# Kernel optimization log

Hardware: AMD Instinct MI355X
Metric: run time of the kernel (lower is better)

Reference implementation:

```python
import jax, jax.numpy as jnp
import numpy as np

N, D, N_SIGMAS = 4096, 128, 75

def _pairwise_sq_dist(x):
    # squared euclidean distances, [N, N]
    sq = jnp.sum(x * x, axis=1)
    d2 = sq[:, None] + sq[None, :] - 2.0 * (x @ x.T)
    return jnp.maximum(d2, 0.0)

def setup_inputs() -> dict:
    key = jax.random.key(0)
    kx, ky = jax.random.split(key)
    x = jax.random.normal(kx, (N, D), dtype=jnp.float32)
    # realistic label kernel: RBF over random 10-dim label embeddings
    y = jax.random.normal(ky, (N, 10), dtype=jnp.float32)
    label_kernel = jnp.exp(-_pairwise_sq_dist(y))
    return {"x": x, "label_kernel": label_kernel}

def reference(x, label_kernel):
    n = x.shape[0]
    d2 = _pairwise_sq_dist(x)              # [N, N] squared distances
    nz = d2 > 0
    # safe sqrt (avoid nan grads on diagonal zeros)
    dist = jnp.where(nz, jnp.sqrt(jnp.where(nz, d2, 1.0)), 0.0)
    # mean of nonzero distances (distance[distance != 0].mean())
    mean_distance = jnp.sum(dist) / jnp.sum(nz).astype(x.dtype)
    lo = 0.1 * mean_distance
    hi = 10.0 * mean_distance
    step = (hi - lo) / N_SIGMAS
    sigmas = lo + step * jnp.arange(N_SIGMAS, dtype=x.dtype)  # np.arange equivalent

    label_norm = jnp.linalg.norm(label_kernel)

    def alignment_loss(sigma):
        K = jnp.exp(-d2 / (sigma * sigma))
        return jnp.sum(K * label_kernel) / (jnp.linalg.norm(K) * label_norm)

    losses = jax.lax.map(alignment_loss, sigmas)   # sequential sigma sweep
    sigma_opt = sigmas[jnp.argmax(losses)]         # first max, like np.argwhere(...).item()

    A = jnp.exp(-d2 / (sigma_opt * sigma_opt)) / n
    return A
```

## Files before the change

kernel.cpp:

```cpp
#include <hip/hip_runtime.h>
#include <hip/hip_bf16.h>

#define NN 4096
#define DD 128
#define NS 75

#define BT 128
#define NBD2 (NN / BT)
#define GRID_D2 (NBD2 * (NBD2 + 1) / 2)

#define SB 64
#define NBSW (NN / SB)
#define NTILES (NBSW * (NBSW + 1) / 2)
#define GRID_SW (NTILES / 2)

typedef float v2f __attribute__((ext_vector_type(2)));
typedef float f32x4 __attribute__((ext_vector_type(4)));
typedef short bf16x8 __attribute__((ext_vector_type(8)));

__device__ __forceinline__ float fexp2(float v) { return __builtin_amdgcn_exp2f(v); }

__device__ __forceinline__ void gload_lds16(const void* g, void* l) {
    __builtin_amdgcn_global_load_lds(
        (const __attribute__((address_space(1))) unsigned int*)g,
        (__attribute__((address_space(3))) unsigned int*)l,
        16, 0, 0);
}

template <int CTRL>
__device__ __forceinline__ float dpp_add(float x) {
    int y = __builtin_amdgcn_update_dpp(0, __float_as_int(x), CTRL, 0xf, 0xf, true);
    return x + __int_as_float(y);
}
__device__ __forceinline__ float wave_sum(float x) {
    x = dpp_add<0x111>(x);
    x = dpp_add<0x112>(x);
    x = dpp_add<0x114>(x);
    x = dpp_add<0x118>(x);
    x = dpp_add<0x142>(x);
    x = dpp_add<0x143>(x);
    return x;
}

__device__ __forceinline__ void tri_decode(int t, int nb, int& bi, int& bj) {
    int b = 0, rem = t;
    while (rem >= nb - b) { rem -= nb - b; ++b; }
    bi = b; bj = b + rem;
}

__device__ __forceinline__ void cvt_split(const float4& v0, const float4& v1,
                                          bf16x8& hi, bf16x8& lo) {
    float f[8] = {v0.x, v0.y, v0.z, v0.w, v1.x, v1.y, v1.z, v1.w};
#pragma unroll
    for (int j = 0; j < 8; ++j) {
        unsigned b = __float_as_uint(f[j]);
        hi[j] = (short)(b >> 16);
        float l = f[j] - __uint_as_float(b & 0xFFFF0000u);
        lo[j] = (short)(__float_as_uint(l) >> 16);
    }
}

__device__ __forceinline__ int coarse_window(const double* KL, const double* KK) {
    double best = -1.0;
    int bk = 0;
    for (int k = 0; k < 25; ++k) {
        double loss = KL[k] / sqrt(KK[k]);
        if (loss > best) { best = loss; bk = k; }
    }
    int wv = 3 * bk - 2;
    if (wv < 0) wv = 0;
    if (wv > NS - 5) wv = NS - 5;
    return wv;
}

#define WS_DSUM 0
#define WS_NZC  8
#define WS_KL   16
#define WS_KK   (16 + 256)
#define WS_SQ   (16 + 512)
#define WS_CSIG (WS_SQ + 4 * NN)

__global__ void k_rowsq(const float* __restrict__ x, float* __restrict__ sq,
                        double* __restrict__ dsum, unsigned long long* __restrict__ nzc) {
    int tid = blockIdx.x * blockDim.x + threadIdx.x;
    if (tid == 0) { *dsum = 0.0; *nzc = 0ull; }
    if (tid < NN) {
        const float4* row = (const float4*)(x + (size_t)tid * DD);
        float s = 0.f;
#pragma unroll
        for (int i = 0; i < DD / 4; ++i) {
            float4 v = row[i];
            s += v.x * v.x + v.y * v.y + v.z * v.z + v.w * v.w;
        }
        sq[tid] = s;
    }
}

__launch_bounds__(256)
__global__ void k_d2(const float* __restrict__ x, const float* __restrict__ sq,
                     float* __restrict__ d2, double* __restrict__ dsum,
                     unsigned long long* __restrict__ nzc) {
    __shared__ double red_d[4];
    __shared__ int red_n[4];

    int bi, bj;
    tri_decode(blockIdx.x, NBD2, bi, bj);
    const int r0 = bi * BT, c0 = bj * BT;
    const int tid = threadIdx.x;
    const int l  = tid & 63, wid = tid >> 6;
    const int wr = wid >> 1, wc = wid & 1;
    const int lr = l & 15;
    const int lk = (l >> 4) * 8;
    const int l4 = (l >> 4) * 4;

    const int ar = r0 + wr * 64 + lr;
    const int br = c0 + wc * 64 + lr;

    f32x4 acc[4][4];
#pragma unroll
    for (int a = 0; a < 4; ++a)
#pragma unroll
        for (int b = 0; b < 4; ++b) acc[a][b] = (f32x4){0.f, 0.f, 0.f, 0.f};

#pragma unroll 1
    for (int kc = 0; kc < 4; ++kc) {
        const int k0 = kc * 32 + lk;
        bf16x8 ah[4], al[4], bh[4], bl[4];
#pragma unroll
        for (int t = 0; t < 4; ++t) {
            const float* pa = x + (size_t)(ar + t * 16) * DD + k0;
            float4 a0 = *(const float4*)pa;
            float4 a1 = *(const float4*)(pa + 4);
            cvt_split(a0, a1, ah[t], al[t]);
            const float* pb = x + (size_t)(br + t * 16) * DD + k0;
            float4 b0 = *(const float4*)pb;
            float4 b1 = *(const float4*)(pb + 4);
            cvt_split(b0, b1, bh[t], bl[t]);
        }
#pragma unroll
        for (int a = 0; a < 4; ++a)
#pragma unroll
            for (int b = 0; b < 4; ++b) {
                acc[a][b] = __builtin_amdgcn_mfma_f32_16x16x32_bf16(ah[a], bh[b], acc[a][b], 0, 0, 0);
                acc[a][b] = __builtin_amdgcn_mfma_f32_16x16x32_bf16(ah[a], bl[b], acc[a][b], 0, 0, 0);
                acc[a][b] = __builtin_amdgcn_mfma_f32_16x16x32_bf16(al[a], bh[b], acc[a][b], 0, 0, 0);
            }
    }

    float myd = 0.f;
    int myn = 0;
#pragma unroll
    for (int a = 0; a < 4; ++a) {
        const int grb = r0 + wr * 64 + a * 16 + l4;
        float4 sqr = *(const float4*)(sq + grb);
        float sr[4] = {sqr.x, sqr.y, sqr.z, sqr.w};
#pragma unroll
        for (int b = 0; b < 4; ++b) {
            const int gc = c0 + wc * 64 + b * 16 + lr;
            const float sc = sq[gc];
            float dv[4];
#pragma unroll
            for (int v = 0; v < 4; ++v) {
                float d = fmaxf(sr[v] + sc - 2.f * acc[a][b][v], 0.f);
                dv[v] = d;
                if (d > 0.f) { myd += sqrtf(d); ++myn; }
                d2[(size_t)(grb + v) * NN + gc] = d;
            }
            if (bi != bj) {
                float4 o = {dv[0], dv[1], dv[2], dv[3]};
                *(float4*)(d2 + (size_t)gc * NN + grb) = o;
            }
        }
    }

    const int w = (bi == bj) ? 1 : 2;
    float sd = wave_sum(myd);
    float sn = wave_sum((float)myn);
    if ((tid & 63) == 63) { red_d[wid] = (double)sd; red_n[wid] = (int)sn; }
    __syncthreads();
    if (tid == 0) {
        double td = red_d[0] + red_d[1] + red_d[2] + red_d[3];
        int tn = red_n[0] + red_n[1] + red_n[2] + red_n[3];
        atomicAdd(dsum, td * (double)w);
        atomicAdd(nzc, (unsigned long long)(tn * w));
    }
}

__global__ void k_sigmas(const double* __restrict__ dsum, const unsigned long long* __restrict__ nzc,
                         float* __restrict__ csig, double* __restrict__ KL, double* __restrict__ KK) {
    int t = threadIdx.x;
    float mean = (float)(*dsum / (double)(*nzc));
    float lo = 0.1f * mean;
    float hi = 10.0f * mean;
    float step = (hi - lo) / (float)NS;
    if (t < NS) {
        float s = lo + step * (float)t;
        csig[t] = (float)(1.4426950408889634 / ((double)s * (double)s));
    }
    if (t < 32) { KL[t] = 0.0; KK[t] = 0.0; }
}

template <bool ADD, int CH, int S0, int STRIDE, int NSLOT>
__device__ __forceinline__ void sweep_phase(const v2f* nd, const v2f* ll,
                                            const float* __restrict__ csig, int off,
                                            double part[4][2 * NSLOT],
                                            int wave, int lane, float w) {
    float c[CH];
#pragma unroll
    for (int s = 0; s < CH; ++s)
        c[s] = __int_as_float(__builtin_amdgcn_readfirstlane(
                   __float_as_int(csig[off + STRIDE * (S0 + s)])));
    v2f akl[CH], akk[CH];
#pragma unroll
    for (int s = 0; s < CH; ++s) { akl[s] = (v2f){0.f, 0.f}; akk[s] = (v2f){0.f, 0.f}; }

#pragma unroll
    for (int e = 0; e < 8; ++e) {
        v2f ndv = nd[e], L = ll[e];
#pragma unroll
        for (int s = 0; s < CH; ++s) {
            v2f arg = ndv * c[s];
            v2f K = {fexp2(arg.x), fexp2(arg.y)};
            akl[s] = __builtin_elementwise_fma(K, L, akl[s]);
            akk[s] = __builtin_elementwise_fma(K, K, akk[s]);
        }
    }

#pragma unroll
    for (int s = 0; s < CH; ++s) {
        float v1 = wave_sum(akl[s].x + akl[s].y);
        float v2 = wave_sum(akk[s].x + akk[s].y);
        if (lane == 63) {
            if (ADD) {
                part[wave][S0 + s]         += (double)(v1 * w);
                part[wave][NSLOT + S0 + s] += (double)(v2 * w);
            } else {
                part[wave][S0 + s]         = (double)(v1 * w);
                part[wave][NSLOT + S0 + s] = (double)(v2 * w);
            }
        }
    }
}

__device__ __forceinline__ void sweep_load_direct(const float* __restrict__ d2,
                                                  const float* __restrict__ lk,
                                                  int r0, int c0, v2f* nd, v2f* ll) {
    const int rr = threadIdx.x >> 4;
    const int c4 = (threadIdx.x & 15) * 4;
#pragma unroll
    for (int it = 0; it < 4; ++it) {
        size_t off = (size_t)(r0 + rr + 16 * it) * NN + c0 + c4;
        float4 dv = *(const float4*)(d2 + off);
        float4 lv = *(const float4*)(lk + off);
        nd[it * 2 + 0] = (v2f){-dv.x, -dv.y};
        nd[it * 2 + 1] = (v2f){-dv.z, -dv.w};
        ll[it * 2 + 0] = (v2f){lv.x, lv.y};
        ll[it * 2 + 1] = (v2f){lv.z, lv.w};
    }
}

__device__ __forceinline__ void sweep_prefetch(const float* __restrict__ d2,
                                               const float* __restrict__ lk,
                                               int r0, int c0, char* wbuf) {
    const int l = threadIdx.x & 63;
    const int wave4 = (threadIdx.x >> 6) * 4;
    const int rr = wave4 + (l >> 4);
    const int c4 = (l & 15) * 4;
#pragma unroll
    for (int q = 0; q < 4; ++q) {
        size_t off = (size_t)(r0 + rr + 16 * q) * NN + c0 + c4;
        gload_lds16(d2 + off, wbuf + q * 1024);
        gload_lds16(lk + off, wbuf + (4 + q) * 1024);
    }
}

__device__ __forceinline__ void sweep_unpack(const char* wbuf, v2f* nd, v2f* ll) {
    const int l = threadIdx.x & 63;
#pragma unroll
    for (int q = 0; q < 4; ++q) {
        f32x4 dv = *(const f32x4*)(wbuf + q * 1024 + l * 16);
        f32x4 lv = *(const f32x4*)(wbuf + (4 + q) * 1024 + l * 16);
        nd[q * 2 + 0] = (v2f){-dv[0], -dv[1]};
        nd[q * 2 + 1] = (v2f){-dv[2], -dv[3]};
        ll[q * 2 + 0] = (v2f){lv[0], lv[1]};
        ll[q * 2 + 1] = (v2f){lv[2], lv[3]};
    }
}

__launch_bounds__(256, 3)
__global__ void k_sweep_coarse(const float* __restrict__ d2, const float* __restrict__ lk,
                               const float* __restrict__ csig, double* __restrict__ KL,
                               double* __restrict__ KK) {
    __shared__ char pbuf[4][8192];
    __shared__ double part[4][50];
    const int lane = threadIdx.x & 63, wave = threadIdx.x >> 6;

    int t0 = blockIdx.x * 2, t1 = t0 + 1;
    int bi0, bj0, bi1, bj1;
    tri_decode(t0, NBSW, bi0, bj0);
    tri_decode(t1, NBSW, bi1, bj1);
    const float w0 = (bi0 == bj0) ? 1.f : 2.f;
    const float w1 = (bi1 == bj1) ? 1.f : 2.f;

    sweep_prefetch(d2, lk, bi1 * SB, bj1 * SB, &pbuf[wave][0]);
    v2f nd[8], ll[8];
    sweep_load_direct(d2, lk, bi0 * SB, bj0 * SB, nd, ll);

    sweep_phase<false, 13, 0, 3, 25>(nd, ll, csig, 0, part, wave, lane, w0);
    sweep_phase<false, 12, 13, 3, 25>(nd, ll, csig, 0, part, wave, lane, w0);

    asm volatile("s_waitcnt vmcnt(0)" ::: "memory");
    sweep_unpack(&pbuf[wave][0], nd, ll);

    sweep_phase<true, 13, 0, 3, 25>(nd, ll, csig, 0, part, wave, lane, w1);
    sweep_phase<true, 12, 13, 3, 25>(nd, ll, csig, 0, part, wave, lane, w1);

    __syncthreads();
    const int t = threadIdx.x;
    if (t < 50) {
        double v = part[0][t] + part[1][t] + part[2][t] + part[3][t];
        if (t < 25) atomicAdd(&KL[t], v);
        else        atomicAdd(&KK[t - 25], v);
    }
}

__launch_bounds__(256, 3)
__global__ void k_sweep_refine(const float* __restrict__ d2, const float* __restrict__ lk,
                               const float* __restrict__ csig, double* __restrict__ KL,
                               double* __restrict__ KK) {
    __shared__ char pbuf[4][8192];
    __shared__ double part[4][10];
    __shared__ int w0_sh;
    if (threadIdx.x == 0) w0_sh = coarse_window(KL, KK);
    const int lane = threadIdx.x & 63, wave = threadIdx.x >> 6;

    int t0 = blockIdx.x * 2, t1 = t0 + 1;
    int bi0, bj0, bi1, bj1;
    tri_decode(t0, NBSW, bi0, bj0);
    tri_decode(t1, NBSW, bi1, bj1);
    const float wt0 = (bi0 == bj0) ? 1.f : 2.f;
    const float wt1 = (bi1 == bj1) ? 1.f : 2.f;

    sweep_prefetch(d2, lk, bi1 * SB, bj1 * SB, &pbuf[wave][0]);
    v2f nd[8], ll[8];
    sweep_load_direct(d2, lk, bi0 * SB, bj0 * SB, nd, ll);
    __syncthreads();
    const int s0 = w0_sh;

    sweep_phase<false, 5, 0, 1, 5>(nd, ll, csig, s0, part, wave, lane, wt0);

    asm volatile("s_waitcnt vmcnt(0)" ::: "memory");
    sweep_unpack(&pbuf[wave][0], nd, ll);

    sweep_phase<true, 5, 0, 1, 5>(nd, ll, csig, s0, part, wave, lane, wt1);

    __syncthreads();
    const int t = threadIdx.x;
    if (t < 10) {
        double v = part[0][t] + part[1][t] + part[2][t] + part[3][t];
        if (t < 5) atomicAdd(&KL[25 + t], v);
        else       atomicAdd(&KK[25 + t - 5], v);
    }
}

__launch_bounds__(256)
__global__ void k_final(float* __restrict__ d2, const double* __restrict__ KL,
                        const double* __restrict__ KK, const float* __restrict__ csig) {
    __shared__ float cc_sh;
    if (threadIdx.x == 0) {
        int wv = coarse_window(KL, KK);
        double best = -1.0;
        int bk = 0;
        for (int k = 0; k < 5; ++k) {
            double loss = KL[25 + k] / sqrt(KK[25 + k]);
            if (loss > best) { best = loss; bk = k; }
        }
        cc_sh = csig[wv + bk];
    }
    __syncthreads();
    const float cc = cc_sh;
    const float inv_n = 1.0f / (float)NN;

    int bi, bj;
    tri_decode(blockIdx.x, NBD2, bi, bj);
    const int r0 = bi * BT, c0 = bj * BT;
    const int tx = threadIdx.x & 31, ty = threadIdx.x >> 5;

    float a[16][4];
#pragma unroll
    for (int r = 0; r < 16; ++r) {
        size_t off = (size_t)(r0 + ty * 16 + r) * NN + c0 + tx * 4;
        float4 v = *(const float4*)(d2 + off);
        a[r][0] = fexp2(-v.x * cc) * inv_n;
        a[r][1] = fexp2(-v.y * cc) * inv_n;
        a[r][2] = fexp2(-v.z * cc) * inv_n;
        a[r][3] = fexp2(-v.w * cc) * inv_n;
        float4 o = {a[r][0], a[r][1], a[r][2], a[r][3]};
        *(float4*)(d2 + off) = o;
    }
    if (bi != bj) {
#pragma unroll
        for (int c = 0; c < 4; ++c) {
            size_t base = (size_t)(c0 + tx * 4 + c) * NN + r0 + ty * 16;
            float4 w0 = {a[0][c],  a[1][c],  a[2][c],  a[3][c]};
            float4 w1 = {a[4][c],  a[5][c],  a[6][c],  a[7][c]};
            float4 w2 = {a[8][c],  a[9][c],  a[10][c], a[11][c]};
            float4 w3 = {a[12][c], a[13][c], a[14][c], a[15][c]};
            *(float4*)(d2 + base + 0)  = w0;
            *(float4*)(d2 + base + 4)  = w1;
            *(float4*)(d2 + base + 8)  = w2;
            *(float4*)(d2 + base + 12) = w3;
        }
    }
}

extern "C" void kernel_launch(void* const* d_in, const int* in_sizes, int n_in,
                              void* d_out, int out_size, void* d_ws, size_t ws_size,
                              hipStream_t stream) {
    const float* x  = (const float*)d_in[0];
    const float* lk = (const float*)d_in[1];
    float* out = (float*)d_out;
    char* ws = (char*)d_ws;

    double* dsum = (double*)(ws + WS_DSUM);
    unsigned long long* nzc = (unsigned long long*)(ws + WS_NZC);
    double* KL = (double*)(ws + WS_KL);
    double* KK = (double*)(ws + WS_KK);
    float* sqv  = (float*)(ws + WS_SQ);
    float* csig = (float*)(ws + WS_CSIG);

    hipLaunchKernelGGL(k_rowsq, dim3(NN / 256), dim3(256), 0, stream, x, sqv, dsum, nzc);
    hipLaunchKernelGGL(k_d2, dim3(GRID_D2), dim3(256), 0, stream, x, sqv, out, dsum, nzc);
    hipLaunchKernelGGL(k_sigmas, dim3(1), dim3(128), 0, stream, dsum, nzc, csig, KL, KK);
    hipLaunchKernelGGL(k_sweep_coarse, dim3(GRID_SW), dim3(256), 0, stream, out, lk, csig, KL, KK);
    hipLaunchKernelGGL(k_sweep_refine, dim3(GRID_SW), dim3(256), 0, stream, out, lk, csig, KL, KK);
    hipLaunchKernelGGL(k_final, dim3(GRID_D2), dim3(256), 0, stream, out, KL, KK, csig);
}
```

Baseline: 151.0 us.

## Stage d2 tiles through LDS for coalesced and transposed stores; stream final exp

The d2 kernel now writes its MFMA accumulator tiles into a per-wave LDS staging buffer and reads them back so each lane issues 16-byte row-contiguous global stores. Mirrored (transposed) tiles are also written as contiguous float4 stores, replacing the former scattered scalar stores. The final exponentiation kernel becomes a flat grid-stride elementwise pass over the whole matrix instead of a triangular tile pass with transposed writes. This trades extra LDS traffic and a full-matrix read for better-coalesced global writes.

After: 147.7 us. 2.2% less time.

```diff
diff --git a/kernel.cpp b/kernel.cpp
--- a/kernel.cpp
+++ b/kernel.cpp
@@ -4,6 +4,7 @@
 #define NN 4096
 #define DD 128
 #define NS 75
+#define TOT (NN * NN)
 
 #define BT 128
 #define NBD2 (NN / BT)
@@ -100,6 +101,7 @@
 __global__ void k_d2(const float* __restrict__ x, const float* __restrict__ sq,
                      float* __restrict__ d2, double* __restrict__ dsum,
                      unsigned long long* __restrict__ nzc) {
+    __shared__ float st[4][32][68];
     __shared__ double red_d[4];
     __shared__ int red_n[4];
 
@@ -156,19 +158,42 @@
         float sr[4] = {sqr.x, sqr.y, sqr.z, sqr.w};
 #pragma unroll
         for (int b = 0; b < 4; ++b) {
-            const int gc = c0 + wc * 64 + b * 16 + lr;
-            const float sc = sq[gc];
-            float dv[4];
+            const float sc = sq[c0 + wc * 64 + b * 16 + lr];
 #pragma unroll
             for (int v = 0; v < 4; ++v) {
                 float d = fmaxf(sr[v] + sc - 2.f * acc[a][b][v], 0.f);
-                dv[v] = d;
+                acc[a][b][v] = d;
                 if (d > 0.f) { myd += sqrtf(d); ++myn; }
-                d2[(size_t)(grb + v) * NN + gc] = d;
             }
-            if (bi != bj) {
-                float4 o = {dv[0], dv[1], dv[2], dv[3]};
-                *(float4*)(d2 + (size_t)gc * NN + grb) = o;
+        }
+    }
+
+    const int row0 = r0 + wr * 64, col0 = c0 + wc * 64;
+#pragma unroll
+    for (int p = 0; p < 2; ++p) {
+#pragma unroll
+        for (int ha = 0; ha < 2; ++ha) {
+            const int a = 2 * p + ha;
+#pragma unroll
+            for (int b = 0; b < 4; ++b)
+#pragma unroll
+                for (int v = 0; v < 4; ++v)
+                    st[wid][ha * 16 + l4 + v][b * 16 + lr] = acc[a][b][v];
+        }
+#pragma unroll
+        for (int q = 0; q < 8; ++q) {
+            const int lr2 = q * 4 + (l >> 4);
+            f32x4 vv = *(const f32x4*)&st[wid][lr2][(l & 15) * 4];
+            *(f32x4*)(d2 + (size_t)(row0 + p * 32 + lr2) * NN + col0 + (l & 15) * 4) = vv;
+        }
+        if (bi != bj) {
+#pragma unroll
+            for (int q = 0; q < 8; ++q) {
+                const int tc = q * 8 + (l >> 3);
+                const int trb = (l & 7) * 4;
+                f32x4 vv = {st[wid][trb + 0][tc], st[wid][trb + 1][tc],
+                            st[wid][trb + 2][tc], st[wid][trb + 3][tc]};
+                *(f32x4*)(d2 + (size_t)(col0 + tc) * NN + row0 + p * 32 + trb) = vv;
             }
         }
     }
@@ -380,37 +405,15 @@
     __syncthreads();
     const float cc = cc_sh;
     const float inv_n = 1.0f / (float)NN;
-
-    int bi, bj;
-    tri_decode(blockIdx.x, NBD2, bi, bj);
-    const int r0 = bi * BT, c0 = bj * BT;
-    const int tx = threadIdx.x & 31, ty = threadIdx.x >> 5;
-
-    float a[16][4];
-#pragma unroll
-    for (int r = 0; r < 16; ++r) {
-        size_t off = (size_t)(r0 + ty * 16 + r) * NN + c0 + tx * 4;
-        float4 v = *(const float4*)(d2 + off);
-        a[r][0] = fexp2(-v.x * cc) * inv_n;
-        a[r][1] = fexp2(-v.y * cc) * inv_n;
-        a[r][2] = fexp2(-v.z * cc) * inv_n;
-        a[r][3] = fexp2(-v.w * cc) * inv_n;
-        float4 o = {a[r][0], a[r][1], a[r][2], a[r][3]};
-        *(float4*)(d2 + off) = o;
-    }
-    if (bi != bj) {
-#pragma unroll
-        for (int c = 0; c < 4; ++c) {
-            size_t base = (size_t)(c0 + tx * 4 + c) * NN + r0 + ty * 16;
-            float4 w0 = {a[0][c],  a[1][c],  a[2][c],  a[3][c]};
-            float4 w1 = {a[4][c],  a[5][c],  a[6][c],  a[7][c]};
-            float4 w2 = {a[8][c],  a[9][c],  a[10][c], a[11][c]};
-            float4 w3 = {a[12][c], a[13][c], a[14][c], a[15][c]};
-            *(float4*)(d2 + base + 0)  = w0;
-            *(float4*)(d2 + base + 4)  = w1;
-            *(float4*)(d2 + base + 8)  = w2;
-            *(float4*)(d2 + base + 12) = w3;
-        }
+    const int nthreads = gridDim.x * blockDim.x;
+    float4* p = (float4*)d2;
+    for (int i = blockIdx.x * blockDim.x + threadIdx.x; i < TOT / 4; i += nthreads) {
+        float4 v = p[i];
+        v.x = fexp2(-v.x * cc) * inv_n;
+        v.y = fexp2(-v.y * cc) * inv_n;
+        v.z = fexp2(-v.z * cc) * inv_n;
+        v.w = fexp2(-v.w * cc) * inv_n;
+        p[i] = v;
     }
 }
 
@@ -434,5 +437,5 @@
     hipLaunchKernelGGL(k_sigmas, dim3(1), dim3(128), 0, stream, dsum, nzc, csig, KL, KK);
     hipLaunchKernelGGL(k_sweep_coarse, dim3(GRID_SW), dim3(256), 0, stream, out, lk, csig, KL, KK);
     hipLaunchKernelGGL(k_sweep_refine, dim3(GRID_SW), dim3(256), 0, stream, out, lk, csig, KL, KK);
-    hipLaunchKernelGGL(k_final, dim3(GRID_D2), dim3(256), 0, stream, out, KL, KK, csig);
-}
+    hipLaunchKernelGGL(k_final, dim3(2048), dim3(256), 0, stream, out, KL, KK, csig);
+}
```
